# Kernel tuning notes

Measured on AMD Instinct MI355X. Metric: run time of the kernel, lower is better.

## Reference

```python
import jax, jax.numpy as jnp
import numpy as np

N = 100000
E = 1600000
G = 64  # number of graphs
H = 128
BN_EPS = 1e-5


def setup_inputs() -> dict:
    key = jax.random.key(0)
    ks = jax.random.split(key, 12)
    x = jax.random.normal(ks[0], (N, 3), dtype=jnp.float32)
    edge_index = jax.random.randint(ks[1], (2, E), 0, N, dtype=jnp.int64)
    batch = jnp.sort(jax.random.randint(ks[2], (N,), 0, G, dtype=jnp.int64))
    W1 = jax.random.normal(ks[3], (3, H), dtype=jnp.float32) * 0.3
    W2 = jax.random.normal(ks[4], (H, H), dtype=jnp.float32) * 0.05
    W3 = jax.random.normal(ks[5], (H, H), dtype=jnp.float32) * 0.05
    lin_W = jax.random.normal(ks[6], (H, 2), dtype=jnp.float32) * 0.05
    d = {
        'x': x, 'edge_index': edge_index, 'batch': batch,
        'W1': W1, 'b1': jnp.zeros((H,), jnp.float32),
        'W2': W2, 'b2': jnp.zeros((H,), jnp.float32),
        'W3': W3, 'b3': jnp.zeros((H,), jnp.float32),
        'lin_W': lin_W, 'lin_b': jnp.zeros((2,), jnp.float32),
    }
    for i, kk in zip((1, 2, 3), ks[7:10]):
        d[f'bn{i}_g'] = jnp.ones((H,), jnp.float32)
        d[f'bn{i}_b'] = jnp.zeros((H,), jnp.float32)
        d[f'bn{i}_m'] = jnp.zeros((H,), jnp.float32)
        d[f'bn{i}_v'] = jax.random.uniform(kk, (H,), dtype=jnp.float32, minval=0.5, maxval=1.5)
    return d


def _gcn(x, src, dst, norm, W, b):
    # GCNConv: out = scatter_add(norm * (xW)[src], dst) + b
    h = x @ W
    msg = h[src] * norm[:, None]
    agg = jax.ops.segment_sum(msg, dst, num_segments=N)
    return agg + b


def _bn_eval(x, g, b, m, v):
    return (x - m) * jax.lax.rsqrt(v + BN_EPS) * g + b


def reference(x, edge_index, batch, W1, b1, W2, b2, W3, b3,
              bn1_g, bn1_b, bn1_m, bn1_v,
              bn2_g, bn2_b, bn2_m, bn2_v,
              bn3_g, bn3_b, bn3_m, bn3_v,
              lin_W, lin_b):
    loop = jnp.arange(N, dtype=edge_index.dtype)
    src = jnp.concatenate([edge_index[0], loop])
    dst = jnp.concatenate([edge_index[1], loop])
    # symmetric normalization with self-loops: deg from destination nodes
    deg = jax.ops.segment_sum(jnp.ones_like(dst, dtype=x.dtype), dst, num_segments=N)
    dinv = jnp.where(deg > 0, jax.lax.rsqrt(deg), 0.0)
    norm = dinv[src] * dinv[dst]

    h = jax.nn.relu(_bn_eval(_gcn(x, src, dst, norm, W1, b1), bn1_g, bn1_b, bn1_m, bn1_v))
    h = jax.nn.relu(_bn_eval(_gcn(h, src, dst, norm, W2, b2), bn2_g, bn2_b, bn2_m, bn2_v))
    h = jax.nn.relu(_bn_eval(_gcn(h, src, dst, norm, W3, b3), bn3_g, bn3_b, bn3_m, bn3_v))
    # dropout is identity in eval mode
    sums = jax.ops.segment_sum(h, batch, num_segments=G)
    cnts = jax.ops.segment_sum(jnp.ones((N,), h.dtype), batch, num_segments=G)
    pooled = sums / jnp.maximum(cnts, 1.0)[:, None]
    return pooled @ lin_W + lin_b
```

## Files before the change

### kernel.cpp

```cpp
#include <hip/hip_runtime.h>

#define NN 100000
#define EE 1600000
#define GG 64
#define HH 128
#define BN_EPS 1e-5f

#define CB 782
#define NB 512
#define TILE 3125

typedef unsigned short ushort_t;

static __device__ inline ushort_t f2bf(float f) {
    unsigned u = __float_as_uint(f);
    unsigned r = (u + 0x7FFF + ((u >> 16) & 1)) >> 16;
    return (ushort_t)r;
}
static __device__ inline float bf2f(ushort_t b) {
    return __uint_as_float(((unsigned)b) << 16);
}


__global__ __launch_bounds__(256) void k_hist(const int* __restrict__ ei,
                                              int* __restrict__ histG) {
    __shared__ int h[CB];
    int t = threadIdx.x;
    for (int i = t; i < CB; i += 256) h[i] = 0;
    __syncthreads();
    int e0 = blockIdx.x * TILE;
    for (int i = t; i < TILE; i += 256) {
        int d = ei[EE + e0 + i];
        atomicAdd(&h[d >> 7], 1);
    }
    __syncthreads();
    for (int i = t; i < CB; i += 256) histG[blockIdx.x * CB + i] = h[i];
}

__global__ __launch_bounds__(512) void k_bscan(int* __restrict__ histG,
                                               int* __restrict__ total) {
    __shared__ int sh[NB];
    int t = threadIdx.x;
    int c = blockIdx.x;
    sh[t] = histG[t * CB + c];
    __syncthreads();
    for (int d = 1; d < NB; d <<= 1) {
        int x = (t >= d) ? sh[t - d] : 0;
        __syncthreads();
        sh[t] += x;
        __syncthreads();
    }
    histG[t * CB + c] = (t > 0) ? sh[t - 1] : 0;
    if (t == NB - 1) total[c] = sh[NB - 1];
}

__global__ __launch_bounds__(1024) void k_cbase(const int* __restrict__ total,
                                                int* __restrict__ cbase) {
    __shared__ int sh[1024];
    int t = threadIdx.x;
    sh[t] = (t < CB) ? total[t] : 0;
    __syncthreads();
    for (int d = 1; d < 1024; d <<= 1) {
        int x = (t >= d) ? sh[t - d] : 0;
        __syncthreads();
        sh[t] += x;
        __syncthreads();
    }
    if (t < CB) cbase[t] = (t > 0) ? sh[t - 1] : 0;
    if (t == CB - 1) cbase[CB] = sh[t];
}

__global__ __launch_bounds__(256) void k_cscatter(const int* __restrict__ ei,
                                                  const int* __restrict__ histG,
                                                  const int* __restrict__ cbase,
                                                  int* __restrict__ metaS) {
    __shared__ int base_l[CB];
    __shared__ int cur_l[CB];
    int t = threadIdx.x;
    int b = blockIdx.x;
    for (int i = t; i < CB; i += 256) {
        base_l[i] = cbase[i] + histG[b * CB + i];
        cur_l[i] = 0;
    }
    __syncthreads();
    int e0 = b * TILE;
    for (int i = t; i < TILE; i += 256) {
        int s = ei[e0 + i];
        int d = ei[EE + e0 + i];
        int c = d >> 7;
        int p = base_l[c] + atomicAdd(&cur_l[c], 1);
        metaS[p] = s | ((d & 127) << 17);
    }
}

__global__ __launch_bounds__(256) void k_fine(const int* __restrict__ metaS,
                                              const int* __restrict__ cbase,
                                              int* __restrict__ cnt,
                                              int* __restrict__ offs,
                                              int* __restrict__ col) {
    __shared__ int hist[128];
    __shared__ int scn[128];
    __shared__ int cur[128];
    int t = threadIdx.x;
    int c = blockIdx.x;
    int lo = cbase[c], hi = cbase[c + 1];
    if (t < 128) hist[t] = 0;
    __syncthreads();
    for (int r = lo + t; r < hi; r += 256) atomicAdd(&hist[metaS[r] >> 17], 1);
    __syncthreads();
    if (t < 128) scn[t] = hist[t];
    __syncthreads();
    for (int d = 1; d < 128; d <<= 1) {
        int x = (t >= d && t < 128) ? scn[t - d] : 0;
        __syncthreads();
        if (t < 128) scn[t] += x;
        __syncthreads();
    }
    if (t < 128) {
        int excl = (t > 0) ? scn[t - 1] : 0;
        cur[t] = excl;
        int node = c * 128 + t;
        if (node < NN) {
            cnt[node] = hist[t];
            offs[node] = lo + excl;
        }
    }
    __syncthreads();
    for (int r = lo + t; r < hi; r += 256) {
        int pk = metaS[r];
        int s = pk & 0x1FFFF;
        int idx = atomicAdd(&cur[pk >> 17], 1);
        col[lo + idx] = s;
    }
}

__global__ void k_dinv(const int* __restrict__ cnt, float* __restrict__ dinv) {
    int n = blockIdx.x * blockDim.x + threadIdx.x;
    if (n < NN) dinv[n] = rsqrtf((float)(cnt[n] + 1));
}


__global__ __launch_bounds__(256) void k_aggx(const float* __restrict__ x,
                                              const int* __restrict__ offs,
                                              const int* __restrict__ cnt,
                                              const int* __restrict__ col,
                                              const float* __restrict__ dinv,
                                              float* __restrict__ wgt,
                                              float4* __restrict__ agg) {
    int tid = threadIdx.x;
    int wave = tid >> 6;
    int lane = tid & 63;
    int grp = lane >> 4;
    int l = lane & 15;
    int n = blockIdx.x * 16 + wave * 4 + grp;
    float dv = dinv[n];
    int base = offs[n], cn = cnt[n];
    float a0 = 0.f, a1 = 0.f, a2 = 0.f;
    for (int i = l; i < cn; i += 16) {
        int s = col[base + i];
        float w = dinv[s] * dv;
        wgt[base + i] = w;
        a0 += w * x[s * 3 + 0];
        a1 += w * x[s * 3 + 1];
        a2 += w * x[s * 3 + 2];
    }
#pragma unroll
    for (int off = 8; off >= 1; off >>= 1) {
        a0 += __shfl_xor(a0, off, 16);
        a1 += __shfl_xor(a1, off, 16);
        a2 += __shfl_xor(a2, off, 16);
    }
    if (l == 0) {
        float w0 = dv * dv;
        a0 += w0 * x[n * 3 + 0];
        a1 += w0 * x[n * 3 + 1];
        a2 += w0 * x[n * 3 + 2];
        agg[n] = make_float4(a0, a1, a2, 0.f);
    }
}


#define L1R 16
__global__ void k_l1(const float4* __restrict__ agg,
                     const float* __restrict__ W1,
                     const float* __restrict__ b1, const float* __restrict__ g,
                     const float* __restrict__ bb, const float* __restrict__ m,
                     const float* __restrict__ v, float* __restrict__ out) {
    int c = threadIdx.x;
    float w0 = W1[c], w1 = W1[128 + c], w2 = W1[256 + c];
    float sc = g[c] * rsqrtf(v[c] + BN_EPS);
    float sh = (b1[c] - m[c]) * sc + bb[c];
    int r0 = blockIdx.x * L1R;
    for (int i = 0; i < L1R; i++) {
        int n = r0 + i;
        if (n >= NN) break;
        float4 a = agg[n];
        float t = a.x * w0 + a.y * w1 + a.z * w2;
        t = t * sc + sh;
        out[n * HH + c] = fmaxf(t, 0.f);
    }
}


__global__ __launch_bounds__(256) void k_mm(const float* __restrict__ xin,
                                            const float* __restrict__ W,
                                            ushort_t* __restrict__ outB) {
    __shared__ float xs[64][132];
    int tid = threadIdx.x;
    int tx = tid & 31;
    int ty = tid >> 5;
    int row0 = blockIdx.x * 64;
#pragma unroll
    for (int i = 0; i < 8; i++) {
        int idx4 = i * 256 + tid;
        int r = idx4 >> 5;
        int k4 = (idx4 & 31) * 4;
        int gr = row0 + r;
        float4 vv = (gr < NN) ? *(const float4*)&xin[gr * HH + k4]
                              : make_float4(0.f, 0.f, 0.f, 0.f);
        *(float4*)&xs[r][k4] = vv;
    }
    __syncthreads();
    float acc[8][4];
#pragma unroll
    for (int i = 0; i < 8; i++)
#pragma unroll
        for (int j = 0; j < 4; j++) acc[i][j] = 0.f;

    const float* Wp = W + tx * 4;
#pragma unroll 4
    for (int k = 0; k < 128; k++) {
        float4 w = *(const float4*)&Wp[k * HH];
#pragma unroll
        for (int i = 0; i < 8; i++) {
            float xv = xs[ty * 8 + i][k];
            acc[i][0] += xv * w.x;
            acc[i][1] += xv * w.y;
            acc[i][2] += xv * w.z;
            acc[i][3] += xv * w.w;
        }
    }
#pragma unroll
    for (int i = 0; i < 8; i++) {
        int gr = row0 + ty * 8 + i;
        if (gr < NN) {
            ushort4 o;
            o.x = f2bf(acc[i][0]);
            o.y = f2bf(acc[i][1]);
            o.z = f2bf(acc[i][2]);
            o.w = f2bf(acc[i][3]);
            *(ushort4*)&outB[(size_t)gr * HH + tx * 4] = o;
        }
    }
}


__global__ __launch_bounds__(256) void k_agg(const ushort_t* __restrict__ t,
                                             const int* __restrict__ offs,
                                             const int* __restrict__ cnt,
                                             const int* __restrict__ col,
                                             const float* __restrict__ wgt,
                                             const float* __restrict__ dinv,
                                             const float* __restrict__ bias,
                                             const float* __restrict__ g,
                                             const float* __restrict__ bb,
                                             const float* __restrict__ m,
                                             const float* __restrict__ v,
                                             float* __restrict__ out) {
    int wave = threadIdx.x >> 6;
    int lane = threadIdx.x & 63;
    int half = lane >> 5;
    int l = lane & 31;
    int d = blockIdx.x * 8 + wave * 2 + half;
    int c0 = l * 4;
    float dv = dinv[d];
    float w0 = dv * dv;
    ushort4 selfR = *(const ushort4*)&t[(size_t)d * HH + c0];
    float4 acc;
    acc.x = bf2f(selfR.x) * w0; acc.y = bf2f(selfR.y) * w0;
    acc.z = bf2f(selfR.z) * w0; acc.w = bf2f(selfR.w) * w0;
    int base = offs[d], cn = cnt[d];
    for (int ib = 0; ib < cn; ib += 32) {
        int i = ib + l;
        int s = 0;
        float w = 0.f;
        if (i < cn) {
            s = col[base + i];
            w = wgt[base + i];
        }
        int lim = min(32, cn - ib);
#pragma unroll 4
        for (int j = 0; j < lim; j++) {
            int ss = __shfl(s, j, 32);
            float ww = __shfl(w, j, 32);
            ushort4 tv = *(const ushort4*)&t[(size_t)ss * HH + c0];
            acc.x += ww * bf2f(tv.x);
            acc.y += ww * bf2f(tv.y);
            acc.z += ww * bf2f(tv.z);
            acc.w += ww * bf2f(tv.w);
        }
    }
    float4 gg = *(const float4*)&g[c0];
    float4 vv = *(const float4*)&v[c0];
    float4 mm = *(const float4*)&m[c0];
    float4 bv = *(const float4*)&bb[c0];
    float4 bi = *(const float4*)&bias[c0];
    float sc0 = gg.x * rsqrtf(vv.x + BN_EPS);
    float sc1 = gg.y * rsqrtf(vv.y + BN_EPS);
    float sc2 = gg.z * rsqrtf(vv.z + BN_EPS);
    float sc3 = gg.w * rsqrtf(vv.w + BN_EPS);
    float4 o;
    o.x = fmaxf(acc.x * sc0 + (bi.x - mm.x) * sc0 + bv.x, 0.f);
    o.y = fmaxf(acc.y * sc1 + (bi.y - mm.y) * sc1 + bv.y, 0.f);
    o.z = fmaxf(acc.z * sc2 + (bi.z - mm.z) * sc2 + bv.z, 0.f);
    o.w = fmaxf(acc.w * sc3 + (bi.w - mm.w) * sc3 + bv.w, 0.f);
    *(float4*)&out[d * HH + c0] = o;
}


#define PBLK 2048
__global__ void k_pool(const float* __restrict__ h, const int* __restrict__ batch,
                       float* __restrict__ gsum, int* __restrict__ gcnt) {
    int c = threadIdx.x;
    int per = (NN + PBLK - 1) / PBLK;
    int n0 = blockIdx.x * per;
    int n1 = min(NN, n0 + per);
    if (n0 >= NN) return;
    float acc = 0.f;
    int cur = batch[n0];
    int count = 0;
    for (int n = n0; n < n1; n++) {
        int gr = batch[n];
        if (gr != cur) {
            atomicAdd(&gsum[cur * HH + c], acc);
            if (c == 0) atomicAdd(&gcnt[cur], count);
            acc = 0.f; count = 0; cur = gr;
        }
        acc += h[n * HH + c];
        count++;
    }
    atomicAdd(&gsum[cur * HH + c], acc);
    if (c == 0) atomicAdd(&gcnt[cur], count);
}

__global__ void k_head(const float* __restrict__ gsum, const int* __restrict__ gcnt,
                       const float* __restrict__ linW, const float* __restrict__ linb,
                       float* __restrict__ out) {
    int t = threadIdx.x;
    int gr = t >> 1, j = t & 1;
    float inv = 1.0f / fmaxf((float)gcnt[gr], 1.0f);
    float acc = 0.f;
    for (int c = 0; c < HH; c++) acc += gsum[gr * HH + c] * linW[c * 2 + j];
    out[t] = acc * inv + linb[j];
}


static inline size_t al256(size_t x) { return (x + 255) & ~(size_t)255; }

extern "C" void kernel_launch(void* const* d_in, const int* in_sizes, int n_in,
                              void* d_out, int out_size, void* d_ws, size_t ws_size,
                              hipStream_t stream) {
    const float* x    = (const float*)d_in[0];
    const int*   ei   = (const int*)d_in[1];
    const int*   batch= (const int*)d_in[2];
    const float* W1   = (const float*)d_in[3];
    const float* b1   = (const float*)d_in[4];
    const float* W2   = (const float*)d_in[5];
    const float* b2   = (const float*)d_in[6];
    const float* W3   = (const float*)d_in[7];
    const float* b3   = (const float*)d_in[8];
    const float* linW = (const float*)d_in[9];
    const float* linb = (const float*)d_in[10];
    const float* bn1g = (const float*)d_in[11];
    const float* bn1b = (const float*)d_in[12];
    const float* bn1m = (const float*)d_in[13];
    const float* bn1v = (const float*)d_in[14];
    const float* bn2g = (const float*)d_in[15];
    const float* bn2b = (const float*)d_in[16];
    const float* bn2m = (const float*)d_in[17];
    const float* bn2v = (const float*)d_in[18];
    const float* bn3g = (const float*)d_in[19];
    const float* bn3b = (const float*)d_in[20];
    const float* bn3m = (const float*)d_in[21];
    const float* bn3v = (const float*)d_in[22];
    float* out = (float*)d_out;

    char* ws = (char*)d_ws;
    size_t off = 0;
    int*    histG  = (int*)(ws + off);    off += al256((size_t)NB * CB * 4);
    int*    total  = (int*)(ws + off);    off += al256((size_t)CB * 4);
    int*    cbase  = (int*)(ws + off);    off += al256((size_t)(CB + 1) * 4);
    int*    cnt    = (int*)(ws + off);    off += al256((size_t)NN * 4);
    int*    offs   = (int*)(ws + off);    off += al256((size_t)NN * 4);
    float*  dinv   = (float*)(ws + off);  off += al256((size_t)NN * 4);
    int*    col    = (int*)(ws + off);    off += al256((size_t)EE * 4);
    float*  wgt    = (float*)(ws + off);  off += al256((size_t)EE * 4);
    float4* agg    = (float4*)(ws + off); off += al256((size_t)NN * 16);
    float*  bufA   = (float*)(ws + off);  off += al256((size_t)NN * HH * 4);
    char*   bufB   = (char*)(ws + off);   off += al256((size_t)NN * HH * 4);
    float*  gsum   = (float*)(ws + off);  off += (size_t)GG * HH * 4;
    int*    gcnt   = (int*)(ws + off);    off += al256((size_t)GG * 4);

    int* metaS = (int*)bufB;
    ushort_t* tB = (ushort_t*)bufB;

    hipMemsetAsync(gsum, 0, (size_t)GG * HH * 4 + (size_t)GG * 4, stream);

    int nblkN = (NN + 255) / 256;

    k_hist<<<NB, 256, 0, stream>>>(ei, histG);
    k_bscan<<<CB, NB, 0, stream>>>(histG, total);
    k_cbase<<<1, 1024, 0, stream>>>(total, cbase);
    k_cscatter<<<NB, 256, 0, stream>>>(ei, histG, cbase, metaS);
    k_fine<<<CB, 256, 0, stream>>>(metaS, cbase, cnt, offs, col);
    k_dinv<<<nblkN, 256, 0, stream>>>(cnt, dinv);

    k_aggx<<<NN / 16, 256, 0, stream>>>(x, offs, cnt, col, dinv, wgt, agg);
    k_l1<<<(NN + L1R - 1) / L1R, 128, 0, stream>>>(agg, W1, b1, bn1g, bn1b, bn1m, bn1v, bufA);

    k_mm<<<(NN + 63) / 64, 256, 0, stream>>>(bufA, W2, tB);
    k_agg<<<NN / 8, 256, 0, stream>>>(tB, offs, cnt, col, wgt, dinv,
                                      b2, bn2g, bn2b, bn2m, bn2v, bufA);

    k_mm<<<(NN + 63) / 64, 256, 0, stream>>>(bufA, W3, tB);
    k_agg<<<NN / 8, 256, 0, stream>>>(tB, offs, cnt, col, wgt, dinv,
                                      b3, bn3g, bn3b, bn3m, bn3v, bufA);

    k_pool<<<PBLK, 128, 0, stream>>>(bufA, batch, gsum, gcnt);
    k_head<<<1, 128, 0, stream>>>(gsum, gcnt, linW, linb, out);
}
```

Baseline: 460.6 us.

## Fuse layer-1 into first matmul, store hidden activations as bf16, merge dinv

Layer 1's transform, BN and ReLU are fused into the W2 matmul kernel, so the fp32 100000x128 intermediate is never written or read back. The aggregation output is now stored as bf16 and read as bf16 by the next matmul and the pooling kernel, halving that traffic. The dinv computation moves into k_fine, the histogram uses fewer, larger tiles (NB 256, TILE 6250), and the gather loop is unrolled further. Storing activations in bf16 adds rounding error to the hidden states.

```diff
diff --git a/kernel.cpp b/kernel.cpp
--- a/kernel.cpp
+++ b/kernel.cpp
@@ -7,8 +7,8 @@
 #define BN_EPS 1e-5f
 
 #define CB 782
-#define NB 512
-#define TILE 3125
+#define NB 256
+#define TILE 6250
 
 typedef unsigned short ushort_t;
 
@@ -37,8 +37,8 @@
     for (int i = t; i < CB; i += 256) histG[blockIdx.x * CB + i] = h[i];
 }
 
-__global__ __launch_bounds__(512) void k_bscan(int* __restrict__ histG,
-                                               int* __restrict__ total) {
+__global__ __launch_bounds__(NB) void k_bscan(int* __restrict__ histG,
+                                              int* __restrict__ total) {
     __shared__ int sh[NB];
     int t = threadIdx.x;
     int c = blockIdx.x;
@@ -97,7 +97,8 @@
                                               const int* __restrict__ cbase,
                                               int* __restrict__ cnt,
                                               int* __restrict__ offs,
-                                              int* __restrict__ col) {
+                                              int* __restrict__ col,
+                                              float* __restrict__ dinv) {
     __shared__ int hist[128];
     __shared__ int scn[128];
     __shared__ int cur[128];
@@ -123,6 +124,7 @@
         if (node < NN) {
             cnt[node] = hist[t];
             offs[node] = lo + excl;
+            dinv[node] = rsqrtf((float)(hist[t] + 1));
         }
     }
     __syncthreads();
@@ -132,11 +134,6 @@
         int idx = atomicAdd(&cur[pk >> 17], 1);
         col[lo + idx] = s;
     }
-}
-
-__global__ void k_dinv(const int* __restrict__ cnt, float* __restrict__ dinv) {
-    int n = blockIdx.x * blockDim.x + threadIdx.x;
-    if (n < NN) dinv[n] = rsqrtf((float)(cnt[n] + 1));
 }
 
 
@@ -180,29 +177,77 @@
 }
 
 
-#define L1R 16
-__global__ void k_l1(const float4* __restrict__ agg,
-                     const float* __restrict__ W1,
-                     const float* __restrict__ b1, const float* __restrict__ g,
-                     const float* __restrict__ bb, const float* __restrict__ m,
-                     const float* __restrict__ v, float* __restrict__ out) {
-    int c = threadIdx.x;
-    float w0 = W1[c], w1 = W1[128 + c], w2 = W1[256 + c];
-    float sc = g[c] * rsqrtf(v[c] + BN_EPS);
-    float sh = (b1[c] - m[c]) * sc + bb[c];
-    int r0 = blockIdx.x * L1R;
-    for (int i = 0; i < L1R; i++) {
-        int n = r0 + i;
-        if (n >= NN) break;
-        float4 a = agg[n];
-        float t = a.x * w0 + a.y * w1 + a.z * w2;
-        t = t * sc + sh;
-        out[n * HH + c] = fmaxf(t, 0.f);
-    }
-}
-
-
-__global__ __launch_bounds__(256) void k_mm(const float* __restrict__ xin,
+__global__ __launch_bounds__(256) void k_mml1(const float4* __restrict__ agg,
+                                              const float* __restrict__ W1,
+                                              const float* __restrict__ b1,
+                                              const float* __restrict__ g1,
+                                              const float* __restrict__ bb1,
+                                              const float* __restrict__ m1,
+                                              const float* __restrict__ v1,
+                                              const float* __restrict__ W2,
+                                              ushort_t* __restrict__ outB) {
+    __shared__ float xs[64][132];
+    __shared__ float4 ag[64];
+    int tid = threadIdx.x;
+    int row0 = blockIdx.x * 64;
+    if (tid < 64) {
+        int gr = row0 + tid;
+        ag[tid] = (gr < NN) ? agg[gr] : make_float4(0.f, 0.f, 0.f, 0.f);
+    }
+    __syncthreads();
+    {
+        int c = tid & 127;
+        int rh = tid >> 7;
+        float w0 = W1[c], w1 = W1[128 + c], w2 = W1[256 + c];
+        float sc = g1[c] * rsqrtf(v1[c] + BN_EPS);
+        float sh = (b1[c] - m1[c]) * sc + bb1[c];
+#pragma unroll
+        for (int i = 0; i < 32; i++) {
+            int r = 2 * i + rh;
+            float4 a = ag[r];
+            float t = a.x * w0 + a.y * w1 + a.z * w2;
+            xs[r][c] = fmaxf(t * sc + sh, 0.f);
+        }
+    }
+    __syncthreads();
+
+    int tx = tid & 31;
+    int ty = tid >> 5;
+    float acc[8][4];
+#pragma unroll
+    for (int i = 0; i < 8; i++)
+#pragma unroll
+        for (int j = 0; j < 4; j++) acc[i][j] = 0.f;
+
+    const float* Wp = W2 + tx * 4;
+#pragma unroll 4
+    for (int k = 0; k < 128; k++) {
+        float4 w = *(const float4*)&Wp[k * HH];
+#pragma unroll
+        for (int i = 0; i < 8; i++) {
+            float xv = xs[ty * 8 + i][k];
+            acc[i][0] += xv * w.x;
+            acc[i][1] += xv * w.y;
+            acc[i][2] += xv * w.z;
+            acc[i][3] += xv * w.w;
+        }
+    }
+#pragma unroll
+    for (int i = 0; i < 8; i++) {
+        int gr = row0 + ty * 8 + i;
+        if (gr < NN) {
+            ushort4 o;
+            o.x = f2bf(acc[i][0]);
+            o.y = f2bf(acc[i][1]);
+            o.z = f2bf(acc[i][2]);
+            o.w = f2bf(acc[i][3]);
+            *(ushort4*)&outB[(size_t)gr * HH + tx * 4] = o;
+        }
+    }
+}
+
+
+__global__ __launch_bounds__(256) void k_mm(const ushort_t* __restrict__ xin,
                                             const float* __restrict__ W,
                                             ushort_t* __restrict__ outB) {
     __shared__ float xs[64][132];
@@ -211,14 +256,22 @@
     int ty = tid >> 5;
     int row0 = blockIdx.x * 64;
 #pragma unroll
-    for (int i = 0; i < 8; i++) {
-        int idx4 = i * 256 + tid;
-        int r = idx4 >> 5;
-        int k4 = (idx4 & 31) * 4;
+    for (int i = 0; i < 4; i++) {
+        int idx8 = i * 256 + tid;
+        int r = idx8 >> 4;
+        int k8 = (idx8 & 15) * 8;
         int gr = row0 + r;
-        float4 vv = (gr < NN) ? *(const float4*)&xin[gr * HH + k4]
-                              : make_float4(0.f, 0.f, 0.f, 0.f);
-        *(float4*)&xs[r][k4] = vv;
+        int4 pk = (gr < NN) ? *(const int4*)&xin[(size_t)gr * HH + k8]
+                            : make_int4(0, 0, 0, 0);
+        float* dst = &xs[r][k8];
+        dst[0] = __uint_as_float(((unsigned)pk.x) << 16);
+        dst[1] = __uint_as_float(((unsigned)pk.x) & 0xFFFF0000u);
+        dst[2] = __uint_as_float(((unsigned)pk.y) << 16);
+        dst[3] = __uint_as_float(((unsigned)pk.y) & 0xFFFF0000u);
+        dst[4] = __uint_as_float(((unsigned)pk.z) << 16);
+        dst[5] = __uint_as_float(((unsigned)pk.z) & 0xFFFF0000u);
+        dst[6] = __uint_as_float(((unsigned)pk.w) << 16);
+        dst[7] = __uint_as_float(((unsigned)pk.w) & 0xFFFF0000u);
     }
     __syncthreads();
     float acc[8][4];
@@ -266,7 +319,7 @@
                                              const float* __restrict__ bb,
                                              const float* __restrict__ m,
                                              const float* __restrict__ v,
-                                             float* __restrict__ out) {
+                                             ushort_t* __restrict__ out) {
     int wave = threadIdx.x >> 6;
     int lane = threadIdx.x & 63;
     int half = lane >> 5;
@@ -289,7 +342,7 @@
             w = wgt[base + i];
         }
         int lim = min(32, cn - ib);
-#pragma unroll 4
+#pragma unroll 8
         for (int j = 0; j < lim; j++) {
             int ss = __shfl(s, j, 32);
             float ww = __shfl(w, j, 32);
@@ -309,17 +362,17 @@
     float sc1 = gg.y * rsqrtf(vv.y + BN_EPS);
     float sc2 = gg.z * rsqrtf(vv.z + BN_EPS);
     float sc3 = gg.w * rsqrtf(vv.w + BN_EPS);
-    float4 o;
-    o.x = fmaxf(acc.x * sc0 + (bi.x - mm.x) * sc0 + bv.x, 0.f);
-    o.y = fmaxf(acc.y * sc1 + (bi.y - mm.y) * sc1 + bv.y, 0.f);
-    o.z = fmaxf(acc.z * sc2 + (bi.z - mm.z) * sc2 + bv.z, 0.f);
-    o.w = fmaxf(acc.w * sc3 + (bi.w - mm.w) * sc3 + bv.w, 0.f);
-    *(float4*)&out[d * HH + c0] = o;
+    ushort4 o;
+    o.x = f2bf(fmaxf(acc.x * sc0 + (bi.x - mm.x) * sc0 + bv.x, 0.f));
+    o.y = f2bf(fmaxf(acc.y * sc1 + (bi.y - mm.y) * sc1 + bv.y, 0.f));
+    o.z = f2bf(fmaxf(acc.z * sc2 + (bi.z - mm.z) * sc2 + bv.z, 0.f));
+    o.w = f2bf(fmaxf(acc.w * sc3 + (bi.w - mm.w) * sc3 + bv.w, 0.f));
+    *(ushort4*)&out[(size_t)d * HH + c0] = o;
 }
 
 
 #define PBLK 2048
-__global__ void k_pool(const float* __restrict__ h, const int* __restrict__ batch,
+__global__ void k_pool(const ushort_t* __restrict__ h, const int* __restrict__ batch,
                        float* __restrict__ gsum, int* __restrict__ gcnt) {
     int c = threadIdx.x;
     int per = (NN + PBLK - 1) / PBLK;
@@ -336,7 +389,7 @@
             if (c == 0) atomicAdd(&gcnt[cur], count);
             acc = 0.f; count = 0; cur = gr;
         }
-        acc += h[n * HH + c];
+        acc += bf2f(h[(size_t)n * HH + c]);
         count++;
     }
     atomicAdd(&gsum[cur * HH + c], acc);
@@ -396,36 +449,34 @@
     int*    col    = (int*)(ws + off);    off += al256((size_t)EE * 4);
     float*  wgt    = (float*)(ws + off);  off += al256((size_t)EE * 4);
     float4* agg    = (float4*)(ws + off); off += al256((size_t)NN * 16);
-    float*  bufA   = (float*)(ws + off);  off += al256((size_t)NN * HH * 4);
+    char*   bufA   = (char*)(ws + off);   off += al256((size_t)NN * HH * 2);
     char*   bufB   = (char*)(ws + off);   off += al256((size_t)NN * HH * 4);
     float*  gsum   = (float*)(ws + off);  off += (size_t)GG * HH * 4;
     int*    gcnt   = (int*)(ws + off);    off += al256((size_t)GG * 4);
 
     int* metaS = (int*)bufB;
     ushort_t* tB = (ushort_t*)bufB;
+    ushort_t* hB = (ushort_t*)bufA;
 
     hipMemsetAsync(gsum, 0, (size_t)GG * HH * 4 + (size_t)GG * 4, stream);
-
-    int nblkN = (NN + 255) / 256;
 
     k_hist<<<NB, 256, 0, stream>>>(ei, histG);
     k_bscan<<<CB, NB, 0, stream>>>(histG, total);
     k_cbase<<<1, 1024, 0, stream>>>(total, cbase);
     k_cscatter<<<NB, 256, 0, stream>>>(ei, histG, cbase, metaS);
-    k_fine<<<CB, 256, 0, stream>>>(metaS, cbase, cnt, offs, col);
-    k_dinv<<<nblkN, 256, 0, stream>>>(cnt, dinv);
+    k_fine<<<CB, 256, 0, stream>>>(metaS, cbase, cnt, offs, col, dinv);
 
     k_aggx<<<NN / 16, 256, 0, stream>>>(x, offs, cnt, col, dinv, wgt, agg);
-    k_l1<<<(NN + L1R - 1) / L1R, 128, 0, stream>>>(agg, W1, b1, bn1g, bn1b, bn1m, bn1v, bufA);
-
-    k_mm<<<(NN + 63) / 64, 256, 0, stream>>>(bufA, W2, tB);
+
+    k_mml1<<<(NN + 63) / 64, 256, 0, stream>>>(agg, W1, b1, bn1g, bn1b, bn1m, bn1v,
+                                               W2, tB);
     k_agg<<<NN / 8, 256, 0, stream>>>(tB, offs, cnt, col, wgt, dinv,
-                                      b2, bn2g, bn2b, bn2m, bn2v, bufA);
-
-    k_mm<<<(NN + 63) / 64, 256, 0, stream>>>(bufA, W3, tB);
+                                      b2, bn2g, bn2b, bn2m, bn2v, hB);
+
+    k_mm<<<(NN + 63) / 64, 256, 0, stream>>>(hB, W3, tB);
     k_agg<<<NN / 8, 256, 0, stream>>>(tB, offs, cnt, col, wgt, dinv,
-                                      b3, bn3g, bn3b, bn3m, bn3v, bufA);
-
-    k_pool<<<PBLK, 128, 0, stream>>>(bufA, batch, gsum, gcnt);
+                                      b3, bn3g, bn3b, bn3m, bn3v, hB);
+
+    k_pool<<<PBLK, 128, 0, stream>>>(hB, batch, gsum, gcnt);
     k_head<<<1, 128, 0, stream>>>(gsum, gcnt, linW, linb, out);
 }
```

Measured after the change: 442.8 us. 1.04x faster.
